# Optimization experiments

Hardware: AMD Instinct MI355X
Metric: run time of the kernel (lower is better)

Reference implementation:

```python
import jax, jax.numpy as jnp
import numpy as np

TEMPERATURE = 0.07


def setup_inputs() -> dict:
    key = jax.random.key(0)
    k1, k2 = jax.random.split(key)
    embeddings = jax.random.normal(k1, (8192, 256), dtype=jnp.float32)
    labels = jax.random.randint(k2, (8192,), 0, 1024, dtype=jnp.int64)
    return {"embeddings": embeddings, "labels": labels}


def reference(embeddings, labels):
    b = embeddings.shape[0]
    # L2 normalize rows (torch F.normalize uses eps=1e-12 clamp on the norm)
    norm = jnp.linalg.norm(embeddings, axis=1, keepdims=True)
    en = embeddings / jnp.maximum(norm, 1e-12)
    # [B, B] similarity scaled by temperature
    sim = jnp.matmul(en, en.T) / TEMPERATURE
    # log-softmax over rows (denominator includes the diagonal, as in the original)
    logp = jax.nn.log_softmax(sim, axis=1)
    # positive mask: same label, excluding self
    mask = (labels[:, None] == labels[None, :]) & ~jnp.eye(b, dtype=bool)
    pos_mask = mask.astype(logp.dtype)
    pos_count = pos_mask.sum(axis=1)
    pos_sum = -jnp.sum(logp * pos_mask, axis=1)
    pos_loss = jnp.where(pos_count > 0, pos_sum / jnp.maximum(pos_count, 1.0), 0.0)
    return pos_loss.mean()
```

## Files before the change

### kernel.cpp

```cpp
#include <hip/hip_runtime.h>
#include <hip/hip_bf16.h>

#define B_N 8192
#define D_K 256
#define BM  256
#define BN  32
#define JSPLIT 16
#define JSPAN (B_N / JSPLIT)
#define NTILE (JSPAN / BN)
#define NCLS 1024
#define INVT 14.285714285714286f
#define C1   20.60992907f

typedef __bf16 bf16x8 __attribute__((ext_vector_type(8)));
typedef float  f32x16 __attribute__((ext_vector_type(16)));
typedef float  f32x4  __attribute__((ext_vector_type(4)));

#define AS1 __attribute__((address_space(1)))
#define AS3 __attribute__((address_space(3)))

__device__ __forceinline__ unsigned short f32_to_bf16_rne(float f) {
    unsigned int u = __float_as_uint(f);
    unsigned int r = (u + 0x7FFFu + ((u >> 16) & 1u)) >> 16;
    return (unsigned short)r;
}
__device__ __forceinline__ float bf16_to_f32(unsigned short u) {
    return __uint_as_float(((unsigned int)u) << 16);
}

__global__ void zero_kernel(float* __restrict__ out, int* __restrict__ hist) {
    int g = blockIdx.x * 256 + threadIdx.x;
    if (g < NCLS) hist[g] = 0;
    if (g == 0) out[0] = 0.0f;
}

__global__ void norm_kernel(const float* __restrict__ emb,
                            const int* __restrict__ labels,
                            unsigned short* __restrict__ en,
                            int* __restrict__ hist) {
    const int t = threadIdx.x;
    const int w = t >> 6, l = t & 63;
    const int row = blockIdx.x * 4 + w;
    f32x4 x = *reinterpret_cast<const f32x4*>(emb + (size_t)row * D_K + l * 4);
    float ss = x[0]*x[0] + x[1]*x[1] + x[2]*x[2] + x[3]*x[3];
    #pragma unroll
    for (int m = 1; m < 64; m <<= 1) ss += __shfl_xor(ss, m, 64);
    float sc = 1.0f / fmaxf(sqrtf(ss), 1e-12f);
    ushort4 o;
    o.x = f32_to_bf16_rne(x[0] * sc); o.y = f32_to_bf16_rne(x[1] * sc);
    o.z = f32_to_bf16_rne(x[2] * sc); o.w = f32_to_bf16_rne(x[3] * sc);
    *reinterpret_cast<ushort4*>(en + (size_t)row * D_K + l * 4) = o;
    if (l == 0) atomicAdd(&hist[labels[row]], 1);
}

__launch_bounds__(256, 2)
__global__ void loss_kernel(const unsigned short* __restrict__ en,
                            const int* __restrict__ labels,
                            float* __restrict__ s_part,
                            float* __restrict__ ps_part) {
    __shared__ __align__(16) unsigned short Bls[2][BN * D_K];
    __shared__ __align__(16) int Lab_s[JSPAN];

    const int t  = threadIdx.x;
    const int l  = t & 63;
    const int w  = t >> 6;
    const int ir = l & 31;
    const int h  = l >> 5;

    const int b      = blockIdx.x;
    const int xcd    = b & 7;
    const int local  = b >> 3;
    const int itile  = xcd * 4 + (local & 3);
    const int jsplit = local >> 2;
    const int ibase  = itile * BM;
    const int j0     = jsplit * JSPAN;

    bf16x8 bi0[16], bi1[16];
    {
        const unsigned short* ap0 =
            en + (size_t)(ibase + w * 64 + ir) * D_K + h * 8;
        const unsigned short* ap1 = ap0 + 32 * D_K;
        #pragma unroll
        for (int ks = 0; ks < 16; ++ks) {
            bi0[ks] = *reinterpret_cast<const bf16x8*>(ap0 + ks * 16);
            bi1[ks] = *reinterpret_cast<const bf16x8*>(ap1 + ks * 16);
        }
    }
    const int li0 = labels[ibase + w * 64 + ir];
    const int li1 = labels[ibase + w * 64 + 32 + ir];

    const int srcm = (t & 31) ^ ((t >> 5) & 7);
    const unsigned short* gb =
        en + (size_t)(j0 + (t >> 5)) * D_K + srcm * 8;
    const char* abase0 = (const char*)Bls[0] + (size_t)ir * 512;
    const char* abase1 = (const char*)Bls[1] + (size_t)ir * 512;
    const int xr = (ir & 7) << 4;

    float sA0 = 0.f, sA1 = 0.f, sB0 = 0.f, sB1 = 0.f;
    float pA0 = 0.f, pA1 = 0.f, pB0 = 0.f, pB1 = 0.f;

#define STAGE(bufp, itv)                                                     \
    {                                                                        \
        const unsigned short* gsrc = gb + (size_t)(itv) * (BN * D_K);        \
        char* ldst = (char*)(bufp) + t * 16;                                 \
        _Pragma("unroll")                                                    \
        for (int rd = 0; rd < 4; ++rd)                                       \
            __builtin_amdgcn_global_load_lds(                                \
                (const AS1 void*)(gsrc + rd * 2048),                         \
                (AS3 void*)(ldst + rd * 4096), 16, 0, 0);                    \
    }

#define TILE_COMPUTE(arow_b, itv)                                            \
    {                                                                        \
        int ljv[16];                                                         \
        {                                                                    \
            const int lb = (itv) * BN + h * 4;                               \
            *(int4*)&ljv[0]  = *(const int4*)&Lab_s[lb];                     \
            *(int4*)&ljv[4]  = *(const int4*)&Lab_s[lb + 8];                 \
            *(int4*)&ljv[8]  = *(const int4*)&Lab_s[lb + 16];                \
            *(int4*)&ljv[12] = *(const int4*)&Lab_s[lb + 24];                \
        }                                                                    \
        f32x16 a0, a1;                                                       \
        _Pragma("unroll")                                                    \
        for (int q = 0; q < 16; ++q) { a0[q] = 0.0f; a1[q] = 0.0f; }         \
        __builtin_amdgcn_s_setprio(1);                                       \
        _Pragma("unroll")                                                    \
        for (int ks = 0; ks < 16; ++ks) {                                    \
            const bf16x8 af = *reinterpret_cast<const bf16x8*>(              \
                (arow_b) + ((((ks << 1) | h) << 4) ^ xr));                   \
            a0 = __builtin_amdgcn_mfma_f32_32x32x16_bf16(af, bi0[ks], a0,    \
                                                         0, 0, 0);           \
            a1 = __builtin_amdgcn_mfma_f32_32x32x16_bf16(af, bi1[ks], a1,    \
                                                         0, 0, 0);           \
        }                                                                    \
        __builtin_amdgcn_s_setprio(0);                                       \
        _Pragma("unroll")                                                    \
        for (int q = 0; q < 16; ++q) {                                       \
            float d0 = a0[q], d1 = a1[q];                                    \
            float e0 = __builtin_amdgcn_exp2f(fmaf(d0, C1, -C1));            \
            float e1 = __builtin_amdgcn_exp2f(fmaf(d1, C1, -C1));            \
            if (q & 1) {                                                     \
                sA1 += e0; pA1 += (ljv[q] == li0) ? d0 : 0.0f;               \
                sB1 += e1; pB1 += (ljv[q] == li1) ? d1 : 0.0f;               \
            } else {                                                         \
                sA0 += e0; pA0 += (ljv[q] == li0) ? d0 : 0.0f;               \
                sB0 += e1; pB0 += (ljv[q] == li1) ? d1 : 0.0f;               \
            }                                                                \
        }                                                                    \
    }

    STAGE(Bls[0], 0);
    Lab_s[t]       = labels[j0 + t];
    Lab_s[t + 256] = labels[j0 + t + 256];
    __syncthreads();

    for (int it = 0; it < NTILE; it += 2) {
        if (it + 1 < NTILE) STAGE(Bls[1], it + 1);
        TILE_COMPUTE(abase0, it);
        asm volatile("s_waitcnt vmcnt(0)");
        __syncthreads();
        if (it + 2 < NTILE) STAGE(Bls[0], it + 2);
        TILE_COMPUTE(abase1, it + 1);
        asm volatile("s_waitcnt vmcnt(0)");
        __syncthreads();
    }
#undef STAGE
#undef TILE_COMPUTE

    float sA = sA0 + sA1, pA = pA0 + pA1;
    float sB = sB0 + sB1, pB = pB0 + pB1;
    sA += __shfl_xor(sA, 32, 64);  pA += __shfl_xor(pA, 32, 64);
    sB += __shfl_xor(sB, 32, 64);  pB += __shfl_xor(pB, 32, 64);
    if (h == 0) {
        const size_t base = (size_t)jsplit * B_N + ibase + w * 64 + ir;
        s_part[base]       = sA;
        ps_part[base]      = pA;
        s_part[base + 32]  = sB;
        ps_part[base + 32] = pB;
    }
}

__global__ void final_kernel(const unsigned short* __restrict__ en,
                             const int* __restrict__ labels,
                             const float* __restrict__ s_part,
                             const float* __restrict__ ps_part,
                             const int* __restrict__ hist,
                             float* __restrict__ out) {
    const int t = threadIdx.x, w = t >> 6, l = t & 63;
    const int i = blockIdx.x * 4 + w;
    ushort4 eu = *reinterpret_cast<const ushort4*>(en + (size_t)i * D_K + l * 4);
    float e0 = bf16_to_f32(eu.x), e1 = bf16_to_f32(eu.y),
          e2 = bf16_to_f32(eu.z), e3 = bf16_to_f32(eu.w);
    float self = e0 * e0 + e1 * e1 + e2 * e2 + e3 * e3;
    #pragma unroll
    for (int m = 1; m < 64; m <<= 1) self += __shfl_xor(self, m, 64);
    __shared__ float part[4];
    if (l == 0) {
        float s = 0.f, ps = 0.f;
        #pragma unroll
        for (int k = 0; k < JSPLIT; ++k) {
            s  += s_part[k * B_N + i];
            ps += ps_part[k * B_N + i];
        }
        ps -= self;
        int pc = hist[labels[i]] - 1;
        float loss = (pc > 0) ? (INVT + logf(s)) - ps * INVT / (float)pc : 0.0f;
        part[w] = loss;
    }
    __syncthreads();
    if (t == 0)
        atomicAdd(out, (part[0] + part[1] + part[2] + part[3]) * (1.0f / B_N));
}

extern "C" void kernel_launch(void* const* d_in, const int* in_sizes, int n_in,
                              void* d_out, int out_size, void* d_ws, size_t ws_size,
                              hipStream_t stream) {
    const float* emb    = (const float*)d_in[0];
    const int*   labels = (const int*)d_in[1];
    float*       out    = (float*)d_out;

    unsigned short* en = (unsigned short*)d_ws;
    float* s_part  = (float*)((char*)d_ws + (size_t)B_N * D_K * 2);
    float* ps_part = s_part + JSPLIT * B_N;
    int*   hist    = (int*)(ps_part + JSPLIT * B_N);

    hipLaunchKernelGGL(zero_kernel, dim3(4), dim3(256), 0, stream, out, hist);
    hipLaunchKernelGGL(norm_kernel, dim3(B_N / 4), dim3(256), 0, stream,
                       emb, labels, en, hist);
    hipLaunchKernelGGL(loss_kernel, dim3((B_N / BM) * JSPLIT), dim3(256), 0,
                       stream, en, labels, s_part, ps_part);
    hipLaunchKernelGGL(final_kernel, dim3(B_N / 4), dim3(256), 0, stream,
                       en, labels, s_part, ps_part, hist, out);
}
```

Before: 130.9 us.

## Double j-split, raise occupancy, precompute self-similarity, thread-per-row finalize

Doubles the column split of the loss kernel to 32, which halves each block's span and doubles the grid, and raises launch bounds to 4 blocks per CU for more parallelism and occupancy. Removes the explicit vmcnt waits before barriers. The bf16 self-dot is now computed in the norm kernel and stored, so the final kernel uses one thread per row and reads no embeddings. The trade-off is twice as many partial sums to write and reduce, and register pressure under the tighter launch bound.

```diff
diff --git a/kernel.cpp b/kernel.cpp
--- a/kernel.cpp
+++ b/kernel.cpp
@@ -5,7 +5,7 @@
 #define D_K 256
 #define BM  256
 #define BN  32
-#define JSPLIT 16
+#define JSPLIT 32
 #define JSPAN (B_N / JSPLIT)
 #define NTILE (JSPAN / BN)
 #define NCLS 1024
@@ -37,7 +37,8 @@
 __global__ void norm_kernel(const float* __restrict__ emb,
                             const int* __restrict__ labels,
                             unsigned short* __restrict__ en,
-                            int* __restrict__ hist) {
+                            int* __restrict__ hist,
+                            float* __restrict__ self_arr) {
     const int t = threadIdx.x;
     const int w = t >> 6, l = t & 63;
     const int row = blockIdx.x * 4 + w;
@@ -50,10 +51,18 @@
     o.x = f32_to_bf16_rne(x[0] * sc); o.y = f32_to_bf16_rne(x[1] * sc);
     o.z = f32_to_bf16_rne(x[2] * sc); o.w = f32_to_bf16_rne(x[3] * sc);
     *reinterpret_cast<ushort4*>(en + (size_t)row * D_K + l * 4) = o;
-    if (l == 0) atomicAdd(&hist[labels[row]], 1);
-}
-
-__launch_bounds__(256, 2)
+    float y0 = bf16_to_f32(o.x), y1 = bf16_to_f32(o.y),
+          y2 = bf16_to_f32(o.z), y3 = bf16_to_f32(o.w);
+    float s2 = y0*y0 + y1*y1 + y2*y2 + y3*y3;
+    #pragma unroll
+    for (int m = 1; m < 64; m <<= 1) s2 += __shfl_xor(s2, m, 64);
+    if (l == 0) {
+        self_arr[row] = s2;
+        atomicAdd(&hist[labels[row]], 1);
+    }
+}
+
+__launch_bounds__(256, 4)
 __global__ void loss_kernel(const unsigned short* __restrict__ en,
                             const int* __restrict__ labels,
                             float* __restrict__ s_part,
@@ -150,18 +159,15 @@
     }
 
     STAGE(Bls[0], 0);
-    Lab_s[t]       = labels[j0 + t];
-    Lab_s[t + 256] = labels[j0 + t + 256];
+    Lab_s[t & (JSPAN - 1)] = labels[j0 + (t & (JSPAN - 1))];
     __syncthreads();
 
     for (int it = 0; it < NTILE; it += 2) {
         if (it + 1 < NTILE) STAGE(Bls[1], it + 1);
         TILE_COMPUTE(abase0, it);
-        asm volatile("s_waitcnt vmcnt(0)");
         __syncthreads();
         if (it + 2 < NTILE) STAGE(Bls[0], it + 2);
         TILE_COMPUTE(abase1, it + 1);
-        asm volatile("s_waitcnt vmcnt(0)");
         __syncthreads();
     }
 #undef STAGE
@@ -180,33 +186,27 @@
     }
 }
 
-__global__ void final_kernel(const unsigned short* __restrict__ en,
-                             const int* __restrict__ labels,
+__global__ void final_kernel(const int* __restrict__ labels,
                              const float* __restrict__ s_part,
                              const float* __restrict__ ps_part,
+                             const float* __restrict__ self_arr,
                              const int* __restrict__ hist,
                              float* __restrict__ out) {
-    const int t = threadIdx.x, w = t >> 6, l = t & 63;
-    const int i = blockIdx.x * 4 + w;
-    ushort4 eu = *reinterpret_cast<const ushort4*>(en + (size_t)i * D_K + l * 4);
-    float e0 = bf16_to_f32(eu.x), e1 = bf16_to_f32(eu.y),
-          e2 = bf16_to_f32(eu.z), e3 = bf16_to_f32(eu.w);
-    float self = e0 * e0 + e1 * e1 + e2 * e2 + e3 * e3;
+    const int t = threadIdx.x;
+    const int i = blockIdx.x * 256 + t;
+    float s = 0.f, ps = 0.f;
+    #pragma unroll 8
+    for (int k = 0; k < JSPLIT; ++k) {
+        s  += s_part[(size_t)k * B_N + i];
+        ps += ps_part[(size_t)k * B_N + i];
+    }
+    ps -= self_arr[i];
+    int pc = hist[labels[i]] - 1;
+    float loss = (pc > 0) ? (INVT + logf(s)) - ps * INVT / (float)pc : 0.0f;
     #pragma unroll
-    for (int m = 1; m < 64; m <<= 1) self += __shfl_xor(self, m, 64);
+    for (int m = 1; m < 64; m <<= 1) loss += __shfl_xor(loss, m, 64);
     __shared__ float part[4];
-    if (l == 0) {
-        float s = 0.f, ps = 0.f;
-        #pragma unroll
-        for (int k = 0; k < JSPLIT; ++k) {
-            s  += s_part[k * B_N + i];
-            ps += ps_part[k * B_N + i];
-        }
-        ps -= self;
-        int pc = hist[labels[i]] - 1;
-        float loss = (pc > 0) ? (INVT + logf(s)) - ps * INVT / (float)pc : 0.0f;
-        part[w] = loss;
-    }
+    if ((t & 63) == 0) part[t >> 6] = loss;
     __syncthreads();
     if (t == 0)
         atomicAdd(out, (part[0] + part[1] + part[2] + part[3]) * (1.0f / B_N));
@@ -221,14 +221,15 @@
 
     unsigned short* en = (unsigned short*)d_ws;
     float* s_part  = (float*)((char*)d_ws + (size_t)B_N * D_K * 2);
-    float* ps_part = s_part + JSPLIT * B_N;
-    int*   hist    = (int*)(ps_part + JSPLIT * B_N);
+    float* ps_part = s_part + (size_t)JSPLIT * B_N;
+    int*   hist    = (int*)(ps_part + (size_t)JSPLIT * B_N);
+    float* self_arr = (float*)(hist + NCLS);
 
     hipLaunchKernelGGL(zero_kernel, dim3(4), dim3(256), 0, stream, out, hist);
     hipLaunchKernelGGL(norm_kernel, dim3(B_N / 4), dim3(256), 0, stream,
-                       emb, labels, en, hist);
+                       emb, labels, en, hist, self_arr);
     hipLaunchKernelGGL(loss_kernel, dim3((B_N / BM) * JSPLIT), dim3(256), 0,
                        stream, en, labels, s_part, ps_part);
-    hipLaunchKernelGGL(final_kernel, dim3(B_N / 4), dim3(256), 0, stream,
-                       en, labels, s_part, ps_part, hist, out);
-}
+    hipLaunchKernelGGL(final_kernel, dim3(B_N / 256), dim3(256), 0, stream,
+                       labels, s_part, ps_part, self_arr, hist, out);
+}
```

Measured after the change: 243.5 us. +86.0%, slower.

## Move positive-pair sums to a sparse label-gather pass, drop histogram kernel

Applied to the files above, without the earlier changes.

Removes the per-element label comparison and positive-sum accumulation from the dense similarity kernel, leaving only the exp-sum. The final kernel now stages all labels in shared memory, finds same-label rows with wave ballots, and computes those few dot products directly, which also yields the positive count and replaces the histogram and zero kernels. The column split doubles to give more blocks, and the explicit vmcnt waits before the barriers are dropped. In exchange, every final-kernel block reloads the full label array, and omitting the explicit waits relies on the barrier to order the async LDS loads.

```diff
diff --git a/kernel.cpp b/kernel.cpp
--- a/kernel.cpp
+++ b/kernel.cpp
@@ -5,10 +5,9 @@
 #define D_K 256
 #define BM  256
 #define BN  32
-#define JSPLIT 16
+#define JSPLIT 32
 #define JSPAN (B_N / JSPLIT)
 #define NTILE (JSPAN / BN)
-#define NCLS 1024
 #define INVT 14.285714285714286f
 #define C1   20.60992907f
 
@@ -28,19 +27,13 @@
     return __uint_as_float(((unsigned int)u) << 16);
 }
 
-__global__ void zero_kernel(float* __restrict__ out, int* __restrict__ hist) {
-    int g = blockIdx.x * 256 + threadIdx.x;
-    if (g < NCLS) hist[g] = 0;
-    if (g == 0) out[0] = 0.0f;
-}
-
 __global__ void norm_kernel(const float* __restrict__ emb,
-                            const int* __restrict__ labels,
                             unsigned short* __restrict__ en,
-                            int* __restrict__ hist) {
+                            float* __restrict__ out) {
     const int t = threadIdx.x;
     const int w = t >> 6, l = t & 63;
     const int row = blockIdx.x * 4 + w;
+    if (blockIdx.x == 0 && t == 0) out[0] = 0.0f;
     f32x4 x = *reinterpret_cast<const f32x4*>(emb + (size_t)row * D_K + l * 4);
     float ss = x[0]*x[0] + x[1]*x[1] + x[2]*x[2] + x[3]*x[3];
     #pragma unroll
@@ -50,16 +43,12 @@
     o.x = f32_to_bf16_rne(x[0] * sc); o.y = f32_to_bf16_rne(x[1] * sc);
     o.z = f32_to_bf16_rne(x[2] * sc); o.w = f32_to_bf16_rne(x[3] * sc);
     *reinterpret_cast<ushort4*>(en + (size_t)row * D_K + l * 4) = o;
-    if (l == 0) atomicAdd(&hist[labels[row]], 1);
 }
 
 __launch_bounds__(256, 2)
 __global__ void loss_kernel(const unsigned short* __restrict__ en,
-                            const int* __restrict__ labels,
-                            float* __restrict__ s_part,
-                            float* __restrict__ ps_part) {
+                            float* __restrict__ s_part) {
     __shared__ __align__(16) unsigned short Bls[2][BN * D_K];
-    __shared__ __align__(16) int Lab_s[JSPAN];
 
     const int t  = threadIdx.x;
     const int l  = t & 63;
@@ -86,8 +75,6 @@
             bi1[ks] = *reinterpret_cast<const bf16x8*>(ap1 + ks * 16);
         }
     }
-    const int li0 = labels[ibase + w * 64 + ir];
-    const int li1 = labels[ibase + w * 64 + 32 + ir];
 
     const int srcm = (t & 31) ^ ((t >> 5) & 7);
     const unsigned short* gb =
@@ -97,7 +84,6 @@
     const int xr = (ir & 7) << 4;
 
     float sA0 = 0.f, sA1 = 0.f, sB0 = 0.f, sB1 = 0.f;
-    float pA0 = 0.f, pA1 = 0.f, pB0 = 0.f, pB1 = 0.f;
 
 #define STAGE(bufp, itv)                                                     \
     {                                                                        \
@@ -110,16 +96,8 @@
                 (AS3 void*)(ldst + rd * 4096), 16, 0, 0);                    \
     }
 
-#define TILE_COMPUTE(arow_b, itv)                                            \
+#define TILE_COMPUTE(arow_b)                                                 \
     {                                                                        \
-        int ljv[16];                                                         \
-        {                                                                    \
-            const int lb = (itv) * BN + h * 4;                               \
-            *(int4*)&ljv[0]  = *(const int4*)&Lab_s[lb];                     \
-            *(int4*)&ljv[4]  = *(const int4*)&Lab_s[lb + 8];                 \
-            *(int4*)&ljv[8]  = *(const int4*)&Lab_s[lb + 16];                \
-            *(int4*)&ljv[12] = *(const int4*)&Lab_s[lb + 24];                \
-        }                                                                    \
         f32x16 a0, a1;                                                       \
         _Pragma("unroll")                                                    \
         for (int q = 0; q < 16; ++q) { a0[q] = 0.0f; a1[q] = 0.0f; }         \
@@ -136,75 +114,93 @@
         __builtin_amdgcn_s_setprio(0);                                       \
         _Pragma("unroll")                                                    \
         for (int q = 0; q < 16; ++q) {                                       \
-            float d0 = a0[q], d1 = a1[q];                                    \
-            float e0 = __builtin_amdgcn_exp2f(fmaf(d0, C1, -C1));            \
-            float e1 = __builtin_amdgcn_exp2f(fmaf(d1, C1, -C1));            \
-            if (q & 1) {                                                     \
-                sA1 += e0; pA1 += (ljv[q] == li0) ? d0 : 0.0f;               \
-                sB1 += e1; pB1 += (ljv[q] == li1) ? d1 : 0.0f;               \
-            } else {                                                         \
-                sA0 += e0; pA0 += (ljv[q] == li0) ? d0 : 0.0f;               \
-                sB0 += e1; pB0 += (ljv[q] == li1) ? d1 : 0.0f;               \
-            }                                                                \
+            float e0 = __builtin_amdgcn_exp2f(fmaf(a0[q], C1, -C1));         \
+            float e1 = __builtin_amdgcn_exp2f(fmaf(a1[q], C1, -C1));         \
+            if (q & 1) { sA1 += e0; sB1 += e1; }                             \
+            else       { sA0 += e0; sB0 += e1; }                             \
         }                                                                    \
     }
 
     STAGE(Bls[0], 0);
-    Lab_s[t]       = labels[j0 + t];
-    Lab_s[t + 256] = labels[j0 + t + 256];
     __syncthreads();
 
     for (int it = 0; it < NTILE; it += 2) {
         if (it + 1 < NTILE) STAGE(Bls[1], it + 1);
-        TILE_COMPUTE(abase0, it);
-        asm volatile("s_waitcnt vmcnt(0)");
+        TILE_COMPUTE(abase0);
         __syncthreads();
         if (it + 2 < NTILE) STAGE(Bls[0], it + 2);
-        TILE_COMPUTE(abase1, it + 1);
-        asm volatile("s_waitcnt vmcnt(0)");
+        TILE_COMPUTE(abase1);
         __syncthreads();
     }
 #undef STAGE
 #undef TILE_COMPUTE
 
-    float sA = sA0 + sA1, pA = pA0 + pA1;
-    float sB = sB0 + sB1, pB = pB0 + pB1;
-    sA += __shfl_xor(sA, 32, 64);  pA += __shfl_xor(pA, 32, 64);
-    sB += __shfl_xor(sB, 32, 64);  pB += __shfl_xor(pB, 32, 64);
+    float sA = sA0 + sA1, sB = sB0 + sB1;
+    sA += __shfl_xor(sA, 32, 64);
+    sB += __shfl_xor(sB, 32, 64);
     if (h == 0) {
         const size_t base = (size_t)jsplit * B_N + ibase + w * 64 + ir;
-        s_part[base]       = sA;
-        ps_part[base]      = pA;
-        s_part[base + 32]  = sB;
-        ps_part[base + 32] = pB;
+        s_part[base]      = sA;
+        s_part[base + 32] = sB;
     }
 }
 
 __global__ void final_kernel(const unsigned short* __restrict__ en,
                              const int* __restrict__ labels,
                              const float* __restrict__ s_part,
-                             const float* __restrict__ ps_part,
-                             const int* __restrict__ hist,
                              float* __restrict__ out) {
+    __shared__ __align__(16) int Lab_s[B_N];
+    __shared__ float part[4];
+
     const int t = threadIdx.x, w = t >> 6, l = t & 63;
     const int i = blockIdx.x * 4 + w;
-    ushort4 eu = *reinterpret_cast<const ushort4*>(en + (size_t)i * D_K + l * 4);
-    float e0 = bf16_to_f32(eu.x), e1 = bf16_to_f32(eu.y),
-          e2 = bf16_to_f32(eu.z), e3 = bf16_to_f32(eu.w);
-    float self = e0 * e0 + e1 * e1 + e2 * e2 + e3 * e3;
+
     #pragma unroll
-    for (int m = 1; m < 64; m <<= 1) self += __shfl_xor(self, m, 64);
-    __shared__ float part[4];
+    for (int k = 0; k < B_N / 256; ++k)
+        Lab_s[t + k * 256] = labels[t + k * 256];
+    __syncthreads();
+
+    float ei[4];
+    {
+        ushort4 eu =
+            *reinterpret_cast<const ushort4*>(en + (size_t)i * D_K + l * 4);
+        ei[0] = bf16_to_f32(eu.x); ei[1] = bf16_to_f32(eu.y);
+        ei[2] = bf16_to_f32(eu.z); ei[3] = bf16_to_f32(eu.w);
+    }
+    const int li = Lab_s[i];
+
+    float ps = 0.0f;
+    int   pcnt = 0;
+    for (int c = 0; c < B_N / 64; ++c) {
+        int lj = Lab_s[c * 64 + l];
+        unsigned long long m = __ballot(lj == li);
+        pcnt += __popcll(m);
+        while (m) {
+            int js = __ffsll((long long)m) - 1;
+            m &= m - 1;
+            int j = c * 64 + js;
+            if (j != i) {
+                ushort4 eu = *reinterpret_cast<const ushort4*>(
+                    en + (size_t)j * D_K + l * 4);
+                float d = ei[0] * bf16_to_f32(eu.x)
+                        + ei[1] * bf16_to_f32(eu.y)
+                        + ei[2] * bf16_to_f32(eu.z)
+                        + ei[3] * bf16_to_f32(eu.w);
+                #pragma unroll
+                for (int mm = 1; mm < 64; mm <<= 1) d += __shfl_xor(d, mm, 64);
+                ps += d;
+            }
+        }
+    }
+    pcnt -= 1;
+
+    float sv = (l < 32) ? s_part[(size_t)l * B_N + i] : 0.0f;
+    #pragma unroll
+    for (int mm = 1; mm < 64; mm <<= 1) sv += __shfl_xor(sv, mm, 64);
+
     if (l == 0) {
-        float s = 0.f, ps = 0.f;
-        #pragma unroll
-        for (int k = 0; k < JSPLIT; ++k) {
-            s  += s_part[k * B_N + i];
-            ps += ps_part[k * B_N + i];
-        }
-        ps -= self;
-        int pc = hist[labels[i]] - 1;
-        float loss = (pc > 0) ? (INVT + logf(s)) - ps * INVT / (float)pc : 0.0f;
+        float loss = (pcnt > 0)
+            ? (INVT + logf(sv)) - ps * INVT / (float)pcnt : 0.0f;
         part[w] = loss;
     }
     __syncthreads();
@@ -220,15 +216,12 @@
     float*       out    = (float*)d_out;
 
     unsigned short* en = (unsigned short*)d_ws;
-    float* s_part  = (float*)((char*)d_ws + (size_t)B_N * D_K * 2);
-    float* ps_part = s_part + JSPLIT * B_N;
-    int*   hist    = (int*)(ps_part + JSPLIT * B_N);
-
-    hipLaunchKernelGGL(zero_kernel, dim3(4), dim3(256), 0, stream, out, hist);
+    float* s_part = (float*)((char*)d_ws + (size_t)B_N * D_K * 2);
+
     hipLaunchKernelGGL(norm_kernel, dim3(B_N / 4), dim3(256), 0, stream,
-                       emb, labels, en, hist);
+                       emb, en, out);
     hipLaunchKernelGGL(loss_kernel, dim3((B_N / BM) * JSPLIT), dim3(256), 0,
-                       stream, en, labels, s_part, ps_part);
+                       stream, en, s_part);
     hipLaunchKernelGGL(final_kernel, dim3(B_N / 4), dim3(256), 0, stream,
-                       en, labels, s_part, ps_part, hist, out);
-}
+                       en, labels, s_part, out);
+}
```

Measured after the change: 143.2 us. 1.09x slower.
